# Kernel optimization log

Hardware: AMD Instinct MI355X
Metric: run time of the kernel (lower is better)

The kernel has to match this reference:

```python
import jax, jax.numpy as jnp
from jax import lax
import numpy as np

B, N1, N2 = 4, 2048, 8192
C1, C2, K, F = 128, 64, 15, 128
NSAMPLE = 16
RADIUS = 0.2
KP_EXTEND = 1.0
EXTENT = KP_EXTEND * RADIUS  # area of influence of each kernel point


def setup_inputs() -> dict:
    key = jax.random.key(0)
    k0, k1, k2, k3, k4 = jax.random.split(key, 5)
    xyz1 = jax.random.uniform(k0, (B, N1, 3), dtype=jnp.float32)
    xyz2 = jax.random.uniform(k1, (B, N2, 3), dtype=jnp.float32)
    features1 = jax.random.normal(k2, (B, N1, C1), dtype=jnp.float32)
    features2 = jax.random.normal(k3, (B, N2, C2), dtype=jnp.float32)
    # Kernel points: fixed disposition inside a sphere of RADIUS, first point at
    # center (fixed='center'). Stands in for the offline potential-optimization.
    rng = np.random.RandomState(42)
    dirs = rng.randn(K, 3)
    dirs /= (np.linalg.norm(dirs, axis=1, keepdims=True) + 1e-9)
    rad = rng.rand(K, 1) ** (1.0 / 3.0)
    kp = dirs * rad
    kp[0, :] = 0.0  # fixed center point
    kernel_points = jnp.asarray(kp * RADIUS, dtype=jnp.float32)  # (K, 3)
    # Convolution kernel weights: one C1->F matrix per kernel point.
    W = jax.random.normal(k4, (K, C1, F), dtype=jnp.float32) * 0.05
    return {"xyz1": xyz1, "features1": features1, "xyz2": xyz2,
            "features2": features2, "kernel_points": kernel_points, "W": W}


def reference(xyz1, features1, xyz2, features2, kernel_points, W):
    # kNN search: for each query point in set 2, NSAMPLE nearest points in set 1.
    d2 = jnp.sum((xyz2[:, :, None, :] - xyz1[:, None, :, :]) ** 2, axis=-1)  # (B,N2,N1)
    _, idx = lax.top_k(-d2, NSAMPLE)  # (B, N2, S)
    # Irregular gather of neighbor coordinates and features.
    gather = jax.vmap(lambda arr, i: arr[i])  # per-batch fancy gather
    neigh_xyz = gather(xyz1, idx)        # (B, N2, S, 3)
    neigh_feat = gather(features1, idx)  # (B, N2, S, C1)
    # Neighbor positions relative to the query (center) point.
    rel = neigh_xyz - xyz2[:, :, None, :]  # (B, N2, S, 3)
    # Distances from each neighbor to each kernel point.
    diff = rel[:, :, :, None, :] - kernel_points[None, None, None, :, :]  # (B,N2,S,K,3)
    sq = jnp.sum(diff * diff, axis=-1)                                    # (B,N2,S,K)
    dist = jnp.sqrt(jnp.maximum(sq, 1e-12))
    # Linear kernel-point influence, aggregation_mode='sum'.
    weights = jax.nn.relu(1.0 - dist / EXTENT)  # (B, N2, S, K)
    # Weighted aggregation of neighbor features per kernel point.
    wf = jnp.einsum('bnsk,bnsc->bnkc', weights, neigh_feat)  # (B, N2, K, C1)
    # Kernel point convolution: per-kernel-point linear map, summed over K.
    out = jnp.einsum('bnkc,kcf->bnf', wf, W)  # (B, N2, F)
    out = jax.nn.relu(out)
    # Feature propagation: concat with skip features of set 2 (use_xyz=False).
    return jnp.concatenate([out, features2], axis=-1)  # (B, N2, F + C2)
```

## Files before the change

### kernel.cpp

```cpp
#include <hip/hip_runtime.h>

#define B 4
#define N1 2048
#define N2 8192
#define C1 128
#define C2 64
#define K 15
#define F 128
#define S 16

__global__ __launch_bounds__(512) void knn_kernel(
    const float* __restrict__ xyz1, const float* __restrict__ xyz2,
    unsigned short* __restrict__ nn_idx) {
#pragma clang fp contract(off)
  __shared__ float s_cd[16][522];
  __shared__ unsigned short s_ci[16][522];
  const int b = blockIdx.y;
  const int q0 = blockIdx.x * 16;
  const int tid = threadIdx.x;

  const float* p1 = xyz1 + (size_t)b * N1 * 3;

  const int wv = tid >> 6;
  const int lane = tid & 63;
  const int q = lane & 15;
  const int sub = lane >> 4;
  const float* p2 = xyz2 + ((size_t)b * N2 + q0 + q) * 3;
  const float qx = p2[0], qy = p2[1], qz = p2[2];

  float bd[S];
  int bi[S];
#pragma unroll
  for (int j = 0; j < S; ++j) { bd[j] = 3.4e38f; bi[j] = 0x7fffffff; }

  const int i0 = wv * 256 + sub;
  for (int ii = 0; ii < 64; ++ii) {
    const int i = i0 + (ii << 2);
    float x = p1[i * 3 + 0];
    float y = p1[i * 3 + 1];
    float z = p1[i * 3 + 2];
    float dx = qx - x;
    float dy = qy - y;
    float dz = qz - z;
    float d = dx * dx;
    d = d + dy * dy;
    d = d + dz * dz;
    if (d < bd[S - 1]) {
      bd[S - 1] = d;
      bi[S - 1] = i;
#pragma unroll
      for (int j = S - 1; j > 0; --j) {
        if (bd[j] < bd[j - 1]) {
          float td = bd[j]; bd[j] = bd[j - 1]; bd[j - 1] = td;
          int ti = bi[j]; bi[j] = bi[j - 1]; bi[j - 1] = ti;
        }
      }
    }
  }
  {
    const int ls = (wv * 4 + sub) * 16;
#pragma unroll
    for (int j = 0; j < S; ++j) {
      s_cd[q][ls + j] = bd[j];
      s_ci[q][ls + j] = (unsigned short)bi[j];
    }
  }
  __syncthreads();

  for (int L = 32; L >= 4; L >>= 1) {
    const int half = L >> 1;
    const int nact = 16 * half;
    const int valid = tid < nact;
    float od[16];
    int oi[16];
    int q2 = 0, m = 0;
    if (valid) {
      q2 = tid / half;
      m = tid - q2 * half;
      int pa = (2 * m) * 16, ea = pa + 16;
      int pb = ea, eb = pb + 16;
#pragma unroll
      for (int j = 0; j < 16; ++j) {
        const int a_ok = pa < ea, b_ok = pb < eb;
        const int ra = a_ok ? pa : ea - 1;
        const int rb = b_ok ? pb : eb - 1;
        float da = s_cd[q2][ra];
        int ia = (int)s_ci[q2][ra];
        float db = s_cd[q2][rb];
        int ib = (int)s_ci[q2][rb];
        const int ta = a_ok && (!b_ok || da < db || (da == db && ia < ib));
        od[j] = ta ? da : db;
        oi[j] = ta ? ia : ib;
        pa += ta;
        pb += !ta;
      }
    }
    __syncthreads();
    if (valid) {
#pragma unroll
      for (int j = 0; j < 16; ++j) {
        s_cd[q2][m * 16 + j] = od[j];
        s_ci[q2][m * 16 + j] = (unsigned short)oi[j];
      }
    }
    __syncthreads();
  }

  if (tid < 16) {
    const int q2 = tid;
    int pa = 0, ea = 16, pb = 16, eb = 32;
    unsigned short* op = nn_idx + ((size_t)b * N2 + q0 + q2) * S;
#pragma unroll
    for (int j = 0; j < 16; ++j) {
      const int a_ok = pa < ea, b_ok = pb < eb;
      const int ra = a_ok ? pa : ea - 1;
      const int rb = b_ok ? pb : eb - 1;
      float da = s_cd[q2][ra];
      int ia = (int)s_ci[q2][ra];
      float db = s_cd[q2][rb];
      int ib = (int)s_ci[q2][rb];
      const int ta = a_ok && (!b_ok || da < db || (da == db && ia < ib));
      op[j] = (unsigned short)(ta ? ia : ib);
      pa += ta;
      pb += !ta;
    }
  }
}

__global__ __launch_bounds__(256) void conv_kernel(
    const float* __restrict__ xyz1, const float* __restrict__ feat1,
    const float* __restrict__ xyz2, const float* __restrict__ feat2,
    const float* __restrict__ kp, const float* __restrict__ W,
    const unsigned short* __restrict__ nn_idx, float* __restrict__ out) {
  __shared__ __align__(16) float s_buf[5184];
  int (*s_idx)[S] = (int(*)[S])(s_buf);
  float (*s_rel)[S][3] = (float(*)[S][3])(s_buf + 256);
  float (*s_w)[260] = (float(*)[260])(s_buf + 1024);
  float (*s_red)[16][132] = (float(*)[16][132])(s_buf);
  __shared__ float s_wf[C1][20];
  __shared__ float s_kp[K * 3];

  const int b = blockIdx.y;
  const int q0 = blockIdx.x * 16;
  const int tid = threadIdx.x;

  if (tid < K * 3) s_kp[tid] = kp[tid];
  s_idx[tid >> 4][tid & 15] = (int)nn_idx[((size_t)b * N2 + q0) * S + tid];
  __syncthreads();

  {
    int q = tid >> 4, s = tid & 15;
    int i = s_idx[q][s];
    const float* pn = xyz1 + ((size_t)b * N1 + i) * 3;
    const float* pq = xyz2 + ((size_t)b * N2 + q0 + q) * 3;
    s_rel[q][s][0] = pn[0] - pq[0];
    s_rel[q][s][1] = pn[1] - pq[1];
    s_rel[q][s][2] = pn[2] - pq[2];
  }
  __syncthreads();

  for (int t = tid; t < 16 * S * K; t += 256) {
    int q = t / (S * K);
    int r = t - q * (S * K);
    int s = r / K;
    int k = r - s * K;
    float rx = s_rel[q][s][0] - s_kp[k * 3 + 0];
    float ry = s_rel[q][s][1] - s_kp[k * 3 + 1];
    float rz = s_rel[q][s][2] - s_kp[k * 3 + 2];
    float d = sqrtf(fmaxf(rx * rx + ry * ry + rz * rz, 1e-12f));
    s_w[q][s * 16 + k] = fmaxf(0.0f, 1.0f - d / 0.2f);
  }
  __syncthreads();

  const int q = tid & 15;
  const int cg = tid >> 4;

  float wfr[K][8];
#pragma unroll
  for (int k = 0; k < K; ++k)
#pragma unroll
    for (int j = 0; j < 8; ++j) wfr[k][j] = 0.0f;

  for (int s = 0; s < S; ++s) {
    int i = s_idx[q][s];
    const float4* fp = (const float4*)(feat1 + ((size_t)b * N1 + i) * C1) + cg * 2;
    float4 n0 = fp[0];
    float4 n1 = fp[1];
    const float4* wr = (const float4*)(&s_w[q][s * 16]);
    float4 w0 = wr[0], w1 = wr[1], w2 = wr[2], w3 = wr[3];
    float wk[16] = {w0.x, w0.y, w0.z, w0.w, w1.x, w1.y, w1.z, w1.w,
                    w2.x, w2.y, w2.z, w2.w, w3.x, w3.y, w3.z, w3.w};
#pragma unroll
    for (int k = 0; k < K; ++k) {
      float w = wk[k];
      wfr[k][0] += w * n0.x;
      wfr[k][1] += w * n0.y;
      wfr[k][2] += w * n0.z;
      wfr[k][3] += w * n0.w;
      wfr[k][4] += w * n1.x;
      wfr[k][5] += w * n1.y;
      wfr[k][6] += w * n1.z;
      wfr[k][7] += w * n1.w;
    }
  }

  const int qg = tid >> 7;
  const int cs = (tid >> 5) & 3;
  const int fg = tid & 31;
  float4 acc[8];
#pragma unroll
  for (int qi = 0; qi < 8; ++qi) acc[qi] = make_float4(0.f, 0.f, 0.f, 0.f);

  for (int k = 0; k < K; ++k) {
    __syncthreads();
#pragma unroll
    for (int j = 0; j < 8; ++j) s_wf[cg * 8 + j][q] = wfr[k][j];
    __syncthreads();

    const float4* Wk4 = (const float4*)(W + (size_t)k * C1 * F) + fg;
#pragma unroll 4
    for (int c2 = 0; c2 < 32; ++c2) {
      int c = cs * 32 + c2;
      float4 wa = *(const float4*)(&s_wf[c][qg * 8 + 0]);
      float4 wb = *(const float4*)(&s_wf[c][qg * 8 + 4]);
      float4 w4 = Wk4[c * 32];
      acc[0].x += wa.x * w4.x; acc[0].y += wa.x * w4.y;
      acc[0].z += wa.x * w4.z; acc[0].w += wa.x * w4.w;
      acc[1].x += wa.y * w4.x; acc[1].y += wa.y * w4.y;
      acc[1].z += wa.y * w4.z; acc[1].w += wa.y * w4.w;
      acc[2].x += wa.z * w4.x; acc[2].y += wa.z * w4.y;
      acc[2].z += wa.z * w4.z; acc[2].w += wa.z * w4.w;
      acc[3].x += wa.w * w4.x; acc[3].y += wa.w * w4.y;
      acc[3].z += wa.w * w4.z; acc[3].w += wa.w * w4.w;
      acc[4].x += wb.x * w4.x; acc[4].y += wb.x * w4.y;
      acc[4].z += wb.x * w4.z; acc[4].w += wb.x * w4.w;
      acc[5].x += wb.y * w4.x; acc[5].y += wb.y * w4.y;
      acc[5].z += wb.y * w4.z; acc[5].w += wb.y * w4.w;
      acc[6].x += wb.z * w4.x; acc[6].y += wb.z * w4.y;
      acc[6].z += wb.z * w4.z; acc[6].w += wb.z * w4.w;
      acc[7].x += wb.w * w4.x; acc[7].y += wb.w * w4.y;
      acc[7].z += wb.w * w4.z; acc[7].w += wb.w * w4.w;
    }
  }

  const int qq0 = tid >> 5;
  const int qq1 = 8 + (tid >> 5);
  const int fj = tid & 31;

  if (cs < 2) {
#pragma unroll
    for (int qi = 0; qi < 8; ++qi)
      *(float4*)(&s_red[cs][qg * 8 + qi][fg * 4]) = acc[qi];
  }
  __syncthreads();

  float4 s01_0, s01_1;
  {
    float4 a0 = *(const float4*)&s_red[0][qq0][fj * 4];
    float4 a1 = *(const float4*)&s_red[1][qq0][fj * 4];
    s01_0.x = a0.x + a1.x; s01_0.y = a0.y + a1.y;
    s01_0.z = a0.z + a1.z; s01_0.w = a0.w + a1.w;
    float4 b0 = *(const float4*)&s_red[0][qq1][fj * 4];
    float4 b1 = *(const float4*)&s_red[1][qq1][fj * 4];
    s01_1.x = b0.x + b1.x; s01_1.y = b0.y + b1.y;
    s01_1.z = b0.z + b1.z; s01_1.w = b0.w + b1.w;
  }
  __syncthreads();
  if (cs >= 2) {
#pragma unroll
    for (int qi = 0; qi < 8; ++qi)
      *(float4*)(&s_red[cs - 2][qg * 8 + qi][fg * 4]) = acc[qi];
  }
  __syncthreads();
  {
    float4 a2 = *(const float4*)&s_red[0][qq0][fj * 4];
    float4 a3 = *(const float4*)&s_red[1][qq0][fj * 4];
    float4 v;
    v.x = fmaxf((s01_0.x + a2.x) + a3.x, 0.0f);
    v.y = fmaxf((s01_0.y + a2.y) + a3.y, 0.0f);
    v.z = fmaxf((s01_0.z + a2.z) + a3.z, 0.0f);
    v.w = fmaxf((s01_0.w + a2.w) + a3.w, 0.0f);
    ((float4*)(out + ((size_t)b * N2 + q0 + qq0) * (F + C2)))[fj] = v;
    float4 b2 = *(const float4*)&s_red[0][qq1][fj * 4];
    float4 b3 = *(const float4*)&s_red[1][qq1][fj * 4];
    float4 u;
    u.x = fmaxf((s01_1.x + b2.x) + b3.x, 0.0f);
    u.y = fmaxf((s01_1.y + b2.y) + b3.y, 0.0f);
    u.z = fmaxf((s01_1.z + b2.z) + b3.z, 0.0f);
    u.w = fmaxf((s01_1.w + b2.w) + b3.w, 0.0f);
    ((float4*)(out + ((size_t)b * N2 + q0 + qq1) * (F + C2)))[fj] = u;
  }

  {
    int qq = tid >> 4;
    int j = tid & 15;
    float4 v = ((const float4*)(feat2 + ((size_t)b * N2 + q0 + qq) * C2))[j];
    ((float4*)(out + ((size_t)b * N2 + q0 + qq) * (F + C2) + F))[j] = v;
  }
}

extern "C" void kernel_launch(void* const* d_in, const int* in_sizes, int n_in,
                              void* d_out, int out_size, void* d_ws, size_t ws_size,
                              hipStream_t stream) {
  const float* xyz1 = (const float*)d_in[0];
  const float* feat1 = (const float*)d_in[1];
  const float* xyz2 = (const float*)d_in[2];
  const float* feat2 = (const float*)d_in[3];
  const float* kp = (const float*)d_in[4];
  const float* Wm = (const float*)d_in[5];
  float* out = (float*)d_out;

  unsigned short* nn_idx = (unsigned short*)d_ws;

  knn_kernel<<<dim3(N2 / 16, B), 512, 0, stream>>>(xyz1, xyz2, nn_idx);
  conv_kernel<<<dim3(N2 / 16, B), 256, 0, stream>>>(xyz1, feat1, xyz2, feat2,
                                                    kp, Wm, nn_idx, out);
}
```

Before: 532.6 us.

## Use branchless threshold selection and candidate filtering in kNN kernel

```diff
diff --git a/kernel.cpp b/kernel.cpp
--- a/kernel.cpp
+++ b/kernel.cpp
@@ -9,12 +9,12 @@
 #define F 128
 #define S 16
 
-__global__ __launch_bounds__(512) void knn_kernel(
+__global__ __launch_bounds__(256) void knn_kernel(
     const float* __restrict__ xyz1, const float* __restrict__ xyz2,
     unsigned short* __restrict__ nn_idx) {
 #pragma clang fp contract(off)
-  __shared__ float s_cd[16][522];
-  __shared__ unsigned short s_ci[16][522];
+  __shared__ float s_cd[16][326];
+  __shared__ unsigned short s_ci[16][326];
   const int b = blockIdx.y;
   const int q0 = blockIdx.x * 16;
   const int tid = threadIdx.x;
@@ -25,17 +25,59 @@
   const int lane = tid & 63;
   const int q = lane & 15;
   const int sub = lane >> 4;
+  const int list = wv * 4 + sub;
   const float* p2 = xyz2 + ((size_t)b * N2 + q0 + q) * 3;
   const float qx = p2[0], qy = p2[1], qz = p2[2];
 
+  float vd[16];
+#pragma unroll
+  for (int j = 0; j < 16; ++j) vd[j] = 3.4e38f;
+
+  for (int ii = 0; ii < 128; ++ii) {
+    const int i = list + (ii << 4);
+    float x = p1[i * 3 + 0];
+    float y = p1[i * 3 + 1];
+    float z = p1[i * 3 + 2];
+    float dx = qx - x;
+    float dy = qy - y;
+    float dz = qz - z;
+    float d = dx * dx;
+    d = d + dy * dy;
+    d = d + dz * dz;
+    float nd[16];
+    nd[0] = fminf(vd[0], d);
+#pragma unroll
+    for (int j = 1; j < 16; ++j) nd[j] = fminf(vd[j], fmaxf(vd[j - 1], d));
+#pragma unroll
+    for (int j = 0; j < 16; ++j) vd[j] = nd[j];
+  }
+  const float thr = vd[15];
+
+  int cnt = 0;
+  for (int ii = 0; ii < 128; ++ii) {
+    const int i = list + (ii << 4);
+    float x = p1[i * 3 + 0];
+    float y = p1[i * 3 + 1];
+    float z = p1[i * 3 + 2];
+    float dx = qx - x;
+    float dy = qy - y;
+    float dz = qz - z;
+    float d = dx * dx;
+    d = d + dy * dy;
+    d = d + dz * dz;
+    if (d <= thr) {
+      if (cnt < 20) s_ci[q][list * 20 + cnt] = (unsigned short)i;
+      ++cnt;
+    }
+  }
+  if (cnt > 20) cnt = 20;
+
   float bd[S];
   int bi[S];
 #pragma unroll
   for (int j = 0; j < S; ++j) { bd[j] = 3.4e38f; bi[j] = 0x7fffffff; }
-
-  const int i0 = wv * 256 + sub;
-  for (int ii = 0; ii < 64; ++ii) {
-    const int i = i0 + (ii << 2);
+  for (int t = 0; t < cnt; ++t) {
+    const int i = (int)s_ci[q][list * 20 + t];
     float x = p1[i * 3 + 0];
     float y = p1[i * 3 + 1];
     float z = p1[i * 3 + 2];
@@ -57,8 +99,9 @@
       }
     }
   }
-  {
-    const int ls = (wv * 4 + sub) * 16;
+  __syncthreads();
+  {
+    const int ls = list * 16;
 #pragma unroll
     for (int j = 0; j < S; ++j) {
       s_cd[q][ls + j] = bd[j];
@@ -67,7 +110,7 @@
   }
   __syncthreads();
 
-  for (int L = 32; L >= 4; L >>= 1) {
+  for (int L = 16; L >= 4; L >>= 1) {
     const int half = L >> 1;
     const int nact = 16 * half;
     const int valid = tid < nact;
@@ -312,7 +355,7 @@
 
   unsigned short* nn_idx = (unsigned short*)d_ws;
 
-  knn_kernel<<<dim3(N2 / 16, B), 512, 0, stream>>>(xyz1, xyz2, nn_idx);
+  knn_kernel<<<dim3(N2 / 16, B), 256, 0, stream>>>(xyz1, xyz2, nn_idx);
   conv_kernel<<<dim3(N2 / 16, B), 256, 0, stream>>>(xyz1, feat1, xyz2, feat2,
                                                     kp, Wm, nn_idx, out);
 }
```

Measured after the change: 538.7 us. About the same (+1.1%).
